# Kernel optimization log

Measured on AMD Instinct MI355X. Metric: run time of the kernel, lower is better.

## Reference

```python
import jax, jax.numpy as jnp
import numpy as np

C = 0.01          # Poincare ball curvature 1/100
SQRT_C = 0.1
EPS = 1e-15
BALL_EPS = 4e-3   # geoopt float32 projx boundary epsilon


def _norm(x):
    return jnp.linalg.norm(x, axis=-1, keepdims=True)


def expmap0(u):
    n = jnp.maximum(_norm(u), EPS)
    return jnp.tanh(SQRT_C * n) * u / (SQRT_C * n)


def logmap0(x):
    n = jnp.maximum(_norm(x), EPS)
    t = jnp.clip(SQRT_C * n, -1.0 + 1e-7, 1.0 - 1e-7)
    return jnp.arctanh(t) * x / (SQRT_C * n)


def projx(x):
    maxnorm = (1.0 - BALL_EPS) / SQRT_C
    n = jnp.maximum(_norm(x), EPS)
    return jnp.where(n > maxnorm, x / n * maxnorm, x)


def mobius_matvec(M, x):
    xn = jnp.maximum(_norm(x), EPS)
    mx = x @ M.T
    mxn = jnp.maximum(_norm(mx), EPS)
    t = jnp.clip(SQRT_C * xn, -1.0 + 1e-7, 1.0 - 1e-7)
    res = jnp.tanh(mxn / xn * jnp.arctanh(t)) * mx / (mxn * SQRT_C)
    return jnp.where(jnp.all(mx == 0, axis=-1, keepdims=True), 0.0, res)


def mobius_add(x, y):
    x2 = jnp.sum(x * x, -1, keepdims=True)
    y2 = jnp.sum(y * y, -1, keepdims=True)
    xy = jnp.sum(x * y, -1, keepdims=True)
    num = (1 + 2 * C * xy + C * y2) * x + (1 - C * x2) * y
    den = 1 + 2 * C * xy + C * C * x2 * y2
    return num / jnp.maximum(den, EPS)


def hyp_linear(x, W, b):
    # eval mode: weight dropout is a no-op
    res = projx(mobius_matvec(W, x))
    hb = projx(expmap0(b.reshape(1, -1)))
    return projx(mobius_add(res, hb))


def setup_inputs() -> dict:
    key = jax.random.key(0)
    ks = jax.random.split(key, 10)
    B, S, N, H, HEADS, E = 2, 4, 10000, 64, 4, 160000
    G = B * S
    OC = H // HEADS
    # edges guaranteed to have no self-loops (module removes then re-adds them)
    src = jax.random.randint(ks[0], (G, E), 0, N)
    off = jax.random.randint(ks[1], (G, E), 1, N)
    dst = (src + off) % N
    edge_index = jnp.stack([src, dst], axis=1).astype(jnp.int32)  # [G,2,E]

    def glorot(k, shape, fan):
        a = np.sqrt(6.0 / fan)
        return jax.random.uniform(k, shape, minval=-a, maxval=a, dtype=jnp.float32)

    emb = jax.random.normal(ks[2], (N, H), dtype=jnp.float32)
    att_i = glorot(ks[3], (1, HEADS, OC), HEADS * OC + 1)
    att_j = glorot(ks[4], (1, HEADS, OC), HEADS * OC + 1)
    w1 = glorot(ks[5], (H, OC), H + OC)   # HypLinear(in=16, out=64): weight [out,in]
    b1 = jnp.zeros((H,), jnp.float32)
    w2 = glorot(ks[6], (H, H), H + H)
    b2 = jnp.zeros((H,), jnp.float32)
    history_graphs = jnp.zeros((B, S, N), jnp.float32)  # only shape is used
    return {"history_graphs": history_graphs, "edge_index": edge_index,
            "emb": emb, "att_i": att_i, "att_j": att_j,
            "w1": w1, "b1": b1, "w2": w2, "b2": b2}


def reference(history_graphs, edge_index, emb, att_i, att_j, w1, b1, w2, b2):
    B, S, N = history_graphs.shape
    G = edge_index.shape[0]
    H = emb.shape[1]
    heads = att_i.shape[1]
    oc = H // heads

    # node ids are arange(N) for every (b,s) -> identical features per graph
    x0 = projx(expmap0(emb))   # initHyperX, [N,H]
    xt = logmap0(x0)           # tangent features used by attention, [N,H]

    # add self loops (inputs contain none)
    loops = jnp.broadcast_to(jnp.arange(N, dtype=edge_index.dtype)[None, None, :], (G, 2, N))
    ei = jnp.concatenate([edge_index, loops], axis=-1)  # [G,2,E+N]

    def agg(e):
        src, dst = e[0], e[1]                       # targets (i), sources (j)
        x_i = xt[src].reshape(-1, heads, oc)        # [E2,h,oc]
        x_j = xt[dst].reshape(-1, heads, oc)
        alpha = jnp.sum(x_i * att_i, -1) + jnp.sum(x_j * att_j, -1)  # [E2,h]
        alpha = jax.nn.leaky_relu(alpha, 0.2)
        m = jax.ops.segment_max(alpha, src, num_segments=N)
        a = jnp.exp(alpha - m[src])
        s = jax.ops.segment_sum(a, src, num_segments=N)
        a = a / (s[src] + 1e-16)                    # edge softmax; dropout eval no-op
        sup = jax.ops.segment_sum(x_j * a[..., None], src, num_segments=N)  # [N,h,oc]
        sup = sup.mean(axis=1)                      # concat=False -> head mean, [N,oc]
        return projx(expmap0(sup))

    h = jax.vmap(agg)(ei)                           # [G,N,oc]
    node_emb = h.reshape(B, S, N, oc)[:, -1]        # last timestep, [B,N,oc]

    z = hyp_linear(node_emb, w1, b1)                # 16 -> 64
    z = projx(expmap0(jax.nn.silu(logmap0(z))))     # HypAct(SiLU)
    z = projx(expmap0(logmap0(z)))                  # HypDropout (eval: log/exp round trip)
    z = hyp_linear(z, w2, b2)                       # 64 -> 64
    return z
```

## Files before the change

kernel.cpp:

```cpp
#include <hip/hip_runtime.h>
#include <hip/hip_bf16.h>

#define N_NODES 10000
#define NE 160000
#define CAP 96
#define SQRT_C 0.1f
#define RINV_SQRT_C 10.0f
#define CC 0.01f
#define EPS 1e-15f
#define MAXNORM ((1.0f - 4e-3f) / SQRT_C)
#define RMAXNORM (1.0f / MAXNORM)

__device__ __forceinline__ float frcp(float x) { return __builtin_amdgcn_rcpf(x); }
__device__ __forceinline__ float frsq(float x) { return __builtin_amdgcn_rsqf(x); }

__device__ __forceinline__ float fexp(float x) { return __expf(x); }
__device__ __forceinline__ float ftanh_pos(float x) {
    return 1.0f - 2.0f * frcp(__expf(2.0f * x) + 1.0f);
}
__device__ __forceinline__ float fatanh01(float t) {
    return 0.5f * __logf((1.0f + t) * frcp(1.0f - t));
}

__device__ __forceinline__ float ldf(const void* p, int i, int isbf) {
    return isbf ? __bfloat162float(((const __hip_bfloat16*)p)[i])
                : ((const float*)p)[i];
}

__device__ __forceinline__ int sniff_wave(const void* emb, int tid) {
    unsigned wv = ((const unsigned*)emb)[tid & 63];
    unsigned ex = (wv >> 7) & 0xFFu;
    unsigned long long m = __ballot(ex >= 116u && ex <= 133u);
    return (__popcll(m) >= 32) ? 1 : 0;
}

__device__ __forceinline__ float wsum(float v) {
#pragma unroll
    for (int off = 32; off > 0; off >>= 1) v += __shfl_xor(v, off, 64);
    return v;
}
__device__ __forceinline__ float wmax(float v) {
#pragma unroll
    for (int off = 32; off > 0; off >>= 1) v = fmaxf(v, __shfl_xor(v, off, 64));
    return v;
}

__device__ __forceinline__ float dpp_wsum(float x) {
    int t;
    t = __builtin_amdgcn_update_dpp(0, __float_as_int(x), 0x111, 0xF, 0xF, true);
    x += __int_as_float(t);
    t = __builtin_amdgcn_update_dpp(0, __float_as_int(x), 0x112, 0xF, 0xF, true);
    x += __int_as_float(t);
    t = __builtin_amdgcn_update_dpp(0, __float_as_int(x), 0x114, 0xF, 0xE, true);
    x += __int_as_float(t);
    t = __builtin_amdgcn_update_dpp(0, __float_as_int(x), 0x118, 0xF, 0xC, true);
    x += __int_as_float(t);
    t = __builtin_amdgcn_update_dpp(0, __float_as_int(x), 0x142, 0xA, 0xF, true);
    x += __int_as_float(t);
    t = __builtin_amdgcn_update_dpp(0, __float_as_int(x), 0x143, 0xC, 0xF, true);
    x += __int_as_float(t);
    return __int_as_float(__builtin_amdgcn_readlane(__float_as_int(x), 63));
}

__global__ __launch_bounds__(256) void pre_scatter(const void* __restrict__ emb,
                                                   const void* __restrict__ att_i,
                                                   const void* __restrict__ att_j,
                                                   const void* __restrict__ w1g,
                                                   const void* __restrict__ b1g,
                                                   const void* __restrict__ w2g,
                                                   const void* __restrict__ b2g,
                                                   const int* __restrict__ ei,
                                                   float* __restrict__ xt,
                                                   float* __restrict__ ai,
                                                   float* __restrict__ aj,
                                                   int* __restrict__ cnt,
                                                   unsigned short* __restrict__ bucket,
                                                   int* __restrict__ ovf_cnt,
                                                   unsigned* __restrict__ ovf,
                                                   int* __restrict__ flag,
                                                   float* __restrict__ wf1t,
                                                   float* __restrict__ wf2t,
                                                   float* __restrict__ hb1f,
                                                   float* __restrict__ hb2f,
                                                   float* __restrict__ hbn2) {
    __shared__ int sflag;
    int tid = threadIdx.x;
    int w = tid >> 6, lane = tid & 63;
    if (blockIdx.x < 2500) {
        if (tid < 64) { int s = sniff_wave(emb, tid); if (tid == 0) sflag = s; }
        __syncthreads();
        int isbf = sflag;
        int t = blockIdx.x * 256 + tid;
        int node = t >> 6;
        float u = ldf(emb, node * 64 + lane, isbf);
        float n2c = fmaxf(wsum(u * u), 1e-30f);
        float rn = frsq(n2c);
        float n = n2c * rn;
        float th = ftanh_pos(SQRT_C * n);
        float x0 = th * RINV_SQRT_C * rn * u;
        float x0n = th * RINV_SQRT_C;
        if (x0n > MAXNORM) { x0 *= MAXNORM * frcp(x0n); x0n = MAXNORM; }
        float tc = fminf(SQRT_C * x0n, 1.0f - 1e-7f);
        float xv = fatanh01(tc) * RINV_SQRT_C * frcp(x0n) * x0;
        xt[node * 64 + lane] = xv;
        float pi = xv * ldf(att_i, lane, isbf);
        float pj = xv * ldf(att_j, lane, isbf);
#pragma unroll
        for (int off = 8; off > 0; off >>= 1) {
            pi += __shfl_xor(pi, off, 64);
            pj += __shfl_xor(pj, off, 64);
        }
        if ((lane & 15) == 0) {
            ai[node * 4 + (lane >> 4)] = pi;
            aj[node * 4 + (lane >> 4)] = pj;
        }
    } else if (blockIdx.x < 2813) {
        int e0 = (blockIdx.x - 2500) * 512 + tid;
#pragma unroll
        for (int q = 0; q < 2; ++q) {
            int e = e0 + q * 256;
            if (e >= NE) break;
            int s0 = ei[3 * 2 * NE + e], d0 = ei[3 * 2 * NE + NE + e];
            int s1 = ei[7 * 2 * NE + e], d1 = ei[7 * 2 * NE + NE + e];
            int i0 = s0, i1 = N_NODES + s1;
            int p0 = atomicAdd(&cnt[i0], 1);
            int p1 = atomicAdd(&cnt[i1], 1);
            if (p0 < CAP) bucket[i0 * CAP + p0] = (unsigned short)d0;
            else {
                int oi = atomicAdd(ovf_cnt, 1);
                ovf[oi] = (0u << 28) | ((unsigned)s0 << 14) | (unsigned)d0;
            }
            if (p1 < CAP) bucket[i1 * CAP + p1] = (unsigned short)d1;
            else {
                int oi = atomicAdd(ovf_cnt, 1);
                ovf[oi] = (1u << 28) | ((unsigned)s1 << 14) | (unsigned)d1;
            }
        }
    } else {
        if (tid < 64) { int s = sniff_wave(emb, tid); if (tid == 0) sflag = s; }
        __syncthreads();
        int isbf = sflag;
        if (tid == 0) *flag = isbf;
        for (int i = tid; i < 1024; i += 256) {
            int o = i >> 4, c = i & 15;
            wf1t[c * 64 + o] = ldf(w1g, i, isbf);
        }
        for (int i = tid; i < 4096; i += 256) {
            int o = i >> 6, c = i & 63;
            wf2t[c * 64 + o] = ldf(w2g, i, isbf);
        }
        if (w < 2) {
            const void* bg = w ? b2g : b1g;
            float b = ldf(bg, lane, isbf);
            float n2c = fmaxf(wsum(b * b), 1e-30f);
            float rn = frsq(n2c);
            float n = n2c * rn;
            float th = ftanh_pos(SQRT_C * n);
            float hv = th * RINV_SQRT_C * rn * b;
            float hn = th * RINV_SQRT_C;
            if (hn > MAXNORM) { hv *= MAXNORM * frcp(hn); hn = MAXNORM; }
            (w ? hb2f : hb1f)[lane] = hv;
            if (lane == 0) hbn2[w] = hn * hn;
        }
    }
}

__global__ __launch_bounds__(256) void agg_head(const int* __restrict__ cnt,
                                                const unsigned short* __restrict__ bucket,
                                                const int* __restrict__ ovf_cnt,
                                                const unsigned* __restrict__ ovf,
                                                const float* __restrict__ ai,
                                                const float* __restrict__ aj,
                                                const float* __restrict__ xt,
                                                const float* __restrict__ wf1t,
                                                const float* __restrict__ wf2t,
                                                const float* __restrict__ hb1f,
                                                const float* __restrict__ hb2f,
                                                const float* __restrict__ hbn2,
                                                const int* __restrict__ flag,
                                                void* __restrict__ outv) {
    __shared__ float wlds[4][64 * 4];
    __shared__ int dlds[4][64];
    int w = threadIdx.x >> 6, lane = threadIdx.x & 63;
    int idx = blockIdx.x * 4 + w;
    int slot = (idx >= N_NODES) ? 1 : 0;
    int n = idx - slot * N_NODES;
    int deg = cnt[idx];
    int start = idx * CAP;

    float4 ai4 = *(const float4*)&ai[n * 4];
    float4 aj4n = *(const float4*)&aj[n * 4];
    float ain[4] = {ai4.x, ai4.y, ai4.z, ai4.w};
    float ajn[4] = {aj4n.x, aj4n.y, aj4n.z, aj4n.w};
    int hh = lane >> 4;
    float acc;

    if (deg <= 63) {
        bool act = (lane <= deg);
        int d = (lane < deg) ? (int)bucket[start + lane] : n;
        float4 a4 = act ? *(const float4*)&aj[d * 4] : make_float4(0.f, 0.f, 0.f, 0.f);
        float ajv[4] = {a4.x, a4.y, a4.z, a4.w};
        float eh[4];
#pragma unroll
        for (int h = 0; h < 4; ++h) {
            float a = ain[h] + ajv[h];
            a = (a < 0.0f) ? 0.2f * a : a;
            eh[h] = act ? fexp(a) : 0.0f;
        }
        float sh[4];
#pragma unroll
        for (int h = 0; h < 4; ++h) sh[h] = wsum(eh[h]);
#pragma unroll
        for (int h = 0; h < 4; ++h)
            wlds[w][lane * 4 + h] = eh[h] * (0.25f * frcp(sh[h] + 1e-16f));
        dlds[w][lane] = d;
        int m = deg + 1;
        float s0 = 0.f, s1 = 0.f, s2 = 0.f, s3 = 0.f;
        float s4 = 0.f, s5 = 0.f, s6 = 0.f, s7 = 0.f;
        int e = 0;
        for (; e + 8 <= m; e += 8) {
            int d0 = dlds[w][e],     d1 = dlds[w][e + 1];
            int d2 = dlds[w][e + 2], d3 = dlds[w][e + 3];
            int d4 = dlds[w][e + 4], d5 = dlds[w][e + 5];
            int d6 = dlds[w][e + 6], d7 = dlds[w][e + 7];
            float w0 = wlds[w][(e + 0) * 4 + hh], w1 = wlds[w][(e + 1) * 4 + hh];
            float w2 = wlds[w][(e + 2) * 4 + hh], w3 = wlds[w][(e + 3) * 4 + hh];
            float w4 = wlds[w][(e + 4) * 4 + hh], w5 = wlds[w][(e + 5) * 4 + hh];
            float w6 = wlds[w][(e + 6) * 4 + hh], w7 = wlds[w][(e + 7) * 4 + hh];
            s0 = fmaf(w0, xt[d0 * 64 + lane], s0);
            s1 = fmaf(w1, xt[d1 * 64 + lane], s1);
            s2 = fmaf(w2, xt[d2 * 64 + lane], s2);
            s3 = fmaf(w3, xt[d3 * 64 + lane], s3);
            s4 = fmaf(w4, xt[d4 * 64 + lane], s4);
            s5 = fmaf(w5, xt[d5 * 64 + lane], s5);
            s6 = fmaf(w6, xt[d6 * 64 + lane], s6);
            s7 = fmaf(w7, xt[d7 * 64 + lane], s7);
        }
        for (; e + 4 <= m; e += 4) {
            int d0 = dlds[w][e],     d1 = dlds[w][e + 1];
            int d2 = dlds[w][e + 2], d3 = dlds[w][e + 3];
            float w0 = wlds[w][(e + 0) * 4 + hh], w1 = wlds[w][(e + 1) * 4 + hh];
            float w2 = wlds[w][(e + 2) * 4 + hh], w3 = wlds[w][(e + 3) * 4 + hh];
            s0 = fmaf(w0, xt[d0 * 64 + lane], s0);
            s1 = fmaf(w1, xt[d1 * 64 + lane], s1);
            s2 = fmaf(w2, xt[d2 * 64 + lane], s2);
            s3 = fmaf(w3, xt[d3 * 64 + lane], s3);
        }
        for (; e < m; ++e)
            s0 = fmaf(wlds[w][e * 4 + hh], xt[dlds[w][e] * 64 + lane], s0);
        acc = ((s0 + s1) + (s2 + s3)) + ((s4 + s5) + (s6 + s7));
    } else {
        int bdeg = (deg < CAP) ? deg : CAP;
        int tov = (deg > CAP) ? *ovf_cnt : 0;
        float mh[4];
#pragma unroll
        for (int h = 0; h < 4; ++h) {
            float a = ain[h] + ajn[h];
            mh[h] = (a < 0.0f) ? 0.2f * a : a;
        }
        for (int e = lane; e < bdeg; e += 64) {
            int d = bucket[start + e];
#pragma unroll
            for (int h = 0; h < 4; ++h) {
                float a = ain[h] + aj[d * 4 + h];
                a = (a < 0.0f) ? 0.2f * a : a;
                mh[h] = fmaxf(mh[h], a);
            }
        }
        for (int k = lane; k < tov; k += 64) {
            unsigned pe = ovf[k];
            if ((int)(pe >> 28) == slot && (int)((pe >> 14) & 0x3FFFu) == n) {
                int d = pe & 0x3FFFu;
#pragma unroll
                for (int h = 0; h < 4; ++h) {
                    float a = ain[h] + aj[d * 4 + h];
                    a = (a < 0.0f) ? 0.2f * a : a;
                    mh[h] = fmaxf(mh[h], a);
                }
            }
        }
#pragma unroll
        for (int h = 0; h < 4; ++h) mh[h] = wmax(mh[h]);
        float sh[4] = {0.f, 0.f, 0.f, 0.f};
        if (lane == 0) {
#pragma unroll
            for (int h = 0; h < 4; ++h) {
                float a = ain[h] + ajn[h];
                a = (a < 0.0f) ? 0.2f * a : a;
                sh[h] = fexp(a - mh[h]);
            }
        }
        for (int e = lane; e < bdeg; e += 64) {
            int d = bucket[start + e];
#pragma unroll
            for (int h = 0; h < 4; ++h) {
                float a = ain[h] + aj[d * 4 + h];
                a = (a < 0.0f) ? 0.2f * a : a;
                sh[h] += fexp(a - mh[h]);
            }
        }
        for (int k = lane; k < tov; k += 64) {
            unsigned pe = ovf[k];
            if ((int)(pe >> 28) == slot && (int)((pe >> 14) & 0x3FFFu) == n) {
                int d = pe & 0x3FFFu;
#pragma unroll
                for (int h = 0; h < 4; ++h) {
                    float a = ain[h] + aj[d * 4 + h];
                    a = (a < 0.0f) ? 0.2f * a : a;
                    sh[h] += fexp(a - mh[h]);
                }
            }
        }
#pragma unroll
        for (int h = 0; h < 4; ++h) sh[h] = wsum(sh[h]);
        float scale[4];
#pragma unroll
        for (int h = 0; h < 4; ++h) scale[h] = 0.25f * frcp(sh[h] + 1e-16f);
        float aih = ain[hh], mhh = mh[hh], sch = scale[hh];
        float aself = aih + ajn[hh];
        aself = (aself < 0.0f) ? 0.2f * aself : aself;
        acc = fexp(aself - mhh) * sch * xt[n * 64 + lane];
        for (int e = 0; e < bdeg; ++e) {
            int d = bucket[start + e];
            float a = aih + aj[d * 4 + hh];
            a = (a < 0.0f) ? 0.2f * a : a;
            acc = fmaf(fexp(a - mhh) * sch, xt[d * 64 + lane], acc);
        }
        for (int k = 0; k < tov; ++k) {
            unsigned pe = ovf[k];
            if ((int)(pe >> 28) == slot && (int)((pe >> 14) & 0x3FFFu) == n) {
                int d = pe & 0x3FFFu;
                float a = aih + aj[d * 4 + hh];
                a = (a < 0.0f) ? 0.2f * a : a;
                acc = fmaf(fexp(a - mhh) * sch, xt[d * 64 + lane], acc);
            }
        }
    }
    acc += __shfl_xor(acc, 16, 64);
    acc += __shfl_xor(acc, 32, 64);

    float vl = acc;
    float* vbuf = wlds[w];
    float* zbuf = wlds[w] + 16;
    if (lane < 16) vbuf[lane] = vl;
    int isbf = *flag;
    float y2a = hbn2[0], y2b = hbn2[1];
    float hb1 = hb1f[lane], hb2v = hb2f[lane];

    float n2c = fmaxf(0.25f * dpp_wsum(vl * vl), 1e-30f);
    float rnv = frsq(n2c);
    float nn = n2c * rnv;
    float th0 = ftanh_pos(SQRT_C * nn);
    float s0v = th0 * RINV_SQRT_C * rnv;
    float x0n = th0 * RINV_SQRT_C;
    if (x0n > MAXNORM) { s0v *= MAXNORM * frcp(x0n); x0n = MAXNORM; }

    float a1 = 0.f;
#pragma unroll
    for (int j = 0; j < 4; ++j) {
        const float4 vq = *(const float4*)&vbuf[j * 4];
        a1 = fmaf(wf1t[(4 * j + 0) * 64 + lane], vq.x, a1);
        a1 = fmaf(wf1t[(4 * j + 1) * 64 + lane], vq.y, a1);
        a1 = fmaf(wf1t[(4 * j + 2) * 64 + lane], vq.z, a1);
        a1 = fmaf(wf1t[(4 * j + 3) * 64 + lane], vq.w, a1);
    }
    a1 *= s0v;

    float mxn2 = dpp_wsum(a1 * a1);
    float mxhb = dpp_wsum(a1 * hb1);
    float xn = fmaxf(x0n, EPS);
    float mxc = fmaxf(mxn2, 1e-30f);
    float rmx = frsq(mxc);
    float mxn = mxc * rmx;
    float t = fminf(SQRT_C * xn, 1.0f - 1e-7f);
    float th = ftanh_pos(mxn * frcp(xn) * fatanh01(t));
    float rs = th * RINV_SQRT_C * rmx;
    float rn = th * RINV_SQRT_C;
    if (mxn2 == 0.0f) { rs = 0.f; rn = 0.f; }
    if (rn > MAXNORM) { rs *= MAXNORM * frcp(rn); rn = MAXNORM; }
    float xy = rs * mxhb;
    float x2 = rn * rn;
    float A = 1.0f + 2.0f * CC * xy + CC * y2a;
    float B = 1.0f - CC * x2;
    float rden = frcp(fmaxf(1.0f + 2.0f * CC * xy + CC * CC * x2 * y2a, EPS));
    float z = (A * rs * a1 + B * hb1) * rden;

    float znc = fmaxf(dpp_wsum(z * z), 1e-30f);
    float rzn = frsq(znc);
    float zn = znc * rzn;
    float scz = (zn > MAXNORM) ? MAXNORM * rzn : 1.0f;
    float z1n = fminf(zn, MAXNORM);
    float rz1n = (zn > MAXNORM) ? RMAXNORM : rzn;
    float lg = fatanh01(fminf(SQRT_C * z1n, 1.0f - 1e-7f)) * RINV_SQRT_C * rz1n * scz;
    float u = lg * z;
    u = u * frcp(1.0f + __expf(-u));

    float unc = fmaxf(dpp_wsum(u * u), 1e-30f);
    float run = frsq(unc);
    float un = unc * run;
    float th2 = ftanh_pos(SQRT_C * un);
    float s2 = th2 * RINV_SQRT_C * run;
    float z2n = th2 * RINV_SQRT_C;
    if (z2n > MAXNORM) { s2 *= MAXNORM * frcp(z2n); z2n = MAXNORM; }
    float z2 = u * s2;

    zbuf[lane] = z2;
    float a2 = 0.f;
#pragma unroll
    for (int j = 0; j < 16; ++j) {
        const float4 zq = *(const float4*)&zbuf[j * 4];
        a2 = fmaf(wf2t[(4 * j + 0) * 64 + lane], zq.x, a2);
        a2 = fmaf(wf2t[(4 * j + 1) * 64 + lane], zq.y, a2);
        a2 = fmaf(wf2t[(4 * j + 2) * 64 + lane], zq.z, a2);
        a2 = fmaf(wf2t[(4 * j + 3) * 64 + lane], zq.w, a2);
    }

    float pn2 = dpp_wsum(a2 * a2);
    float ph2 = dpp_wsum(a2 * hb2v);
    float xnb = fmaxf(z2n, EPS);
    float pnc = fmaxf(pn2, 1e-30f);
    float rpx = frsq(pnc);
    float mxnb = pnc * rpx;
    float tb = fminf(SQRT_C * xnb, 1.0f - 1e-7f);
    float thb = ftanh_pos(mxnb * frcp(xnb) * fatanh01(tb));
    float rsb = thb * RINV_SQRT_C * rpx;
    float rnb = thb * RINV_SQRT_C;
    if (pn2 == 0.0f) { rsb = 0.f; rnb = 0.f; }
    if (rnb > MAXNORM) { rsb *= MAXNORM * frcp(rnb); rnb = MAXNORM; }
    float xyb = rsb * ph2;
    float x2b = rnb * rnb;
    float Ab = 1.0f + 2.0f * CC * xyb + CC * y2b;
    float Bb = 1.0f - CC * x2b;
    float rdenb = frcp(fmaxf(1.0f + 2.0f * CC * xyb + CC * CC * x2b * y2b, EPS));
    float zf = (Ab * rsb * a2 + Bb * hb2v) * rdenb;
    float zfc = fmaxf(dpp_wsum(zf * zf), 1e-30f);
    float rzf = frsq(zfc);
    float znf = zfc * rzf;
    float s4 = (znf > MAXNORM) ? MAXNORM * rzf : 1.0f;
    float val = zf * s4;

    if (isbf) ((__hip_bfloat16*)outv)[idx * 64 + lane] = __float2bfloat16(val);
    else      ((float*)outv)[idx * 64 + lane] = val;
}

extern "C" void kernel_launch(void* const* d_in, const int* in_sizes, int n_in,
                              void* d_out, int out_size, void* d_ws, size_t ws_size,
                              hipStream_t stream) {
    const int* ei = (const int*)d_in[1];
    const void* emb   = d_in[2];
    const void* att_i = d_in[3];
    const void* att_j = d_in[4];
    const void* w1 = d_in[5];
    const void* b1 = d_in[6];
    const void* w2 = d_in[7];
    const void* b2 = d_in[8];

    float* ws = (float*)d_ws;
    float* xt    = ws;
    float* ai    = ws + 640000;
    float* aj    = ws + 680000;
    int* cnt     = (int*)(ws + 1040000);
    int* ovf_cnt = (int*)(ws + 1060000);
    unsigned short* bucket = (unsigned short*)(ws + 1060032);
    unsigned* ovf = (unsigned*)(ws + 2020032);
    int* flag     = (int*)(ws + 2340032);
    float* wf1t = ws + 2340064;
    float* wf2t = ws + 2341088;
    float* hb1f = ws + 2345184;
    float* hb2f = ws + 2345248;
    float* hbn2 = ws + 2345312;

    hipMemsetAsync((void*)cnt, 0, (2 * N_NODES + 8) * sizeof(int), stream);
    hipLaunchKernelGGL(pre_scatter, dim3(2814), dim3(256), 0, stream,
                       emb, att_i, att_j, w1, b1, w2, b2, ei,
                       xt, ai, aj, cnt, bucket, ovf_cnt, ovf, flag,
                       wf1t, wf2t, hb1f, hb2f, hbn2);
    hipLaunchKernelGGL(agg_head, dim3(5000), dim3(256), 0, stream,
                       cnt, bucket, ovf_cnt, ovf, ai, aj, xt,
                       wf1t, wf2t, hb1f, hb2f, hbn2, flag, d_out);
}
```

Baseline: 129.4 us.

## Fuse pre-scatter and aggregation into one cooperative kernel with grid sync

Merges the two kernels into a single persistent cooperative kernel. Blocks grid-stride over the old pre-scatter work, meet at a grid-wide barrier, then grid-stride over the aggregation and head work. This removes one kernel launch and the inter-kernel gap, and passes the bf16 flag in shared memory instead of through global memory. In exchange it adds cooperative-launch and grid-sync overhead, an occupancy query on every call, and a grid capped by occupancy, which may reduce parallelism in the gather-heavy phase.

```diff
diff --git a/kernel.cpp b/kernel.cpp
--- a/kernel.cpp
+++ b/kernel.cpp
@@ -1,5 +1,8 @@
 #include <hip/hip_runtime.h>
 #include <hip/hip_bf16.h>
+#include <hip/hip_cooperative_groups.h>
+
+namespace cg = cooperative_groups;
 
 #define N_NODES 10000
 #define NE 160000
@@ -62,215 +65,191 @@
     return __int_as_float(__builtin_amdgcn_readlane(__float_as_int(x), 63));
 }
 
-__global__ __launch_bounds__(256) void pre_scatter(const void* __restrict__ emb,
-                                                   const void* __restrict__ att_i,
-                                                   const void* __restrict__ att_j,
-                                                   const void* __restrict__ w1g,
-                                                   const void* __restrict__ b1g,
-                                                   const void* __restrict__ w2g,
-                                                   const void* __restrict__ b2g,
-                                                   const int* __restrict__ ei,
-                                                   float* __restrict__ xt,
-                                                   float* __restrict__ ai,
-                                                   float* __restrict__ aj,
-                                                   int* __restrict__ cnt,
-                                                   unsigned short* __restrict__ bucket,
-                                                   int* __restrict__ ovf_cnt,
-                                                   unsigned* __restrict__ ovf,
-                                                   int* __restrict__ flag,
-                                                   float* __restrict__ wf1t,
-                                                   float* __restrict__ wf2t,
-                                                   float* __restrict__ hb1f,
-                                                   float* __restrict__ hb2f,
-                                                   float* __restrict__ hbn2) {
+__global__ __launch_bounds__(256, 4) void fused_all(const void* __restrict__ emb,
+                                                    const void* __restrict__ att_i,
+                                                    const void* __restrict__ att_j,
+                                                    const void* __restrict__ w1g,
+                                                    const void* __restrict__ b1g,
+                                                    const void* __restrict__ w2g,
+                                                    const void* __restrict__ b2g,
+                                                    const int* __restrict__ ei,
+                                                    float* __restrict__ xt,
+                                                    float* __restrict__ ai,
+                                                    float* __restrict__ aj,
+                                                    int* __restrict__ cnt,
+                                                    unsigned short* __restrict__ bucket,
+                                                    int* __restrict__ ovf_cnt,
+                                                    unsigned* __restrict__ ovf,
+                                                    float* __restrict__ wf1t,
+                                                    float* __restrict__ wf2t,
+                                                    float* __restrict__ hb1f,
+                                                    float* __restrict__ hb2f,
+                                                    float* __restrict__ hbn2,
+                                                    void* __restrict__ outv) {
+    __shared__ float wlds[4][64 * 4];
+    __shared__ int dlds[4][64];
     __shared__ int sflag;
     int tid = threadIdx.x;
     int w = tid >> 6, lane = tid & 63;
-    if (blockIdx.x < 2500) {
-        if (tid < 64) { int s = sniff_wave(emb, tid); if (tid == 0) sflag = s; }
-        __syncthreads();
-        int isbf = sflag;
-        int t = blockIdx.x * 256 + tid;
-        int node = t >> 6;
-        float u = ldf(emb, node * 64 + lane, isbf);
-        float n2c = fmaxf(wsum(u * u), 1e-30f);
-        float rn = frsq(n2c);
-        float n = n2c * rn;
-        float th = ftanh_pos(SQRT_C * n);
-        float x0 = th * RINV_SQRT_C * rn * u;
-        float x0n = th * RINV_SQRT_C;
-        if (x0n > MAXNORM) { x0 *= MAXNORM * frcp(x0n); x0n = MAXNORM; }
-        float tc = fminf(SQRT_C * x0n, 1.0f - 1e-7f);
-        float xv = fatanh01(tc) * RINV_SQRT_C * frcp(x0n) * x0;
-        xt[node * 64 + lane] = xv;
-        float pi = xv * ldf(att_i, lane, isbf);
-        float pj = xv * ldf(att_j, lane, isbf);
-#pragma unroll
-        for (int off = 8; off > 0; off >>= 1) {
-            pi += __shfl_xor(pi, off, 64);
-            pj += __shfl_xor(pj, off, 64);
-        }
-        if ((lane & 15) == 0) {
-            ai[node * 4 + (lane >> 4)] = pi;
-            aj[node * 4 + (lane >> 4)] = pj;
-        }
-    } else if (blockIdx.x < 2813) {
-        int e0 = (blockIdx.x - 2500) * 512 + tid;
-#pragma unroll
-        for (int q = 0; q < 2; ++q) {
-            int e = e0 + q * 256;
-            if (e >= NE) break;
-            int s0 = ei[3 * 2 * NE + e], d0 = ei[3 * 2 * NE + NE + e];
-            int s1 = ei[7 * 2 * NE + e], d1 = ei[7 * 2 * NE + NE + e];
-            int i0 = s0, i1 = N_NODES + s1;
-            int p0 = atomicAdd(&cnt[i0], 1);
-            int p1 = atomicAdd(&cnt[i1], 1);
-            if (p0 < CAP) bucket[i0 * CAP + p0] = (unsigned short)d0;
-            else {
-                int oi = atomicAdd(ovf_cnt, 1);
-                ovf[oi] = (0u << 28) | ((unsigned)s0 << 14) | (unsigned)d0;
-            }
-            if (p1 < CAP) bucket[i1 * CAP + p1] = (unsigned short)d1;
-            else {
-                int oi = atomicAdd(ovf_cnt, 1);
-                ovf[oi] = (1u << 28) | ((unsigned)s1 << 14) | (unsigned)d1;
-            }
-        }
-    } else {
-        if (tid < 64) { int s = sniff_wave(emb, tid); if (tid == 0) sflag = s; }
-        __syncthreads();
-        int isbf = sflag;
-        if (tid == 0) *flag = isbf;
-        for (int i = tid; i < 1024; i += 256) {
-            int o = i >> 4, c = i & 15;
-            wf1t[c * 64 + o] = ldf(w1g, i, isbf);
-        }
-        for (int i = tid; i < 4096; i += 256) {
-            int o = i >> 6, c = i & 63;
-            wf2t[c * 64 + o] = ldf(w2g, i, isbf);
-        }
-        if (w < 2) {
-            const void* bg = w ? b2g : b1g;
-            float b = ldf(bg, lane, isbf);
-            float n2c = fmaxf(wsum(b * b), 1e-30f);
+
+    if (tid < 64) { int s = sniff_wave(emb, tid); if (tid == 0) sflag = s; }
+    __syncthreads();
+    int isbf = sflag;
+
+    for (int b = blockIdx.x; b < 2814; b += gridDim.x) {
+        if (b < 2500) {
+            int t = b * 256 + tid;
+            int node = t >> 6;
+            float u = ldf(emb, node * 64 + lane, isbf);
+            float n2c = fmaxf(wsum(u * u), 1e-30f);
             float rn = frsq(n2c);
             float n = n2c * rn;
             float th = ftanh_pos(SQRT_C * n);
-            float hv = th * RINV_SQRT_C * rn * b;
-            float hn = th * RINV_SQRT_C;
-            if (hn > MAXNORM) { hv *= MAXNORM * frcp(hn); hn = MAXNORM; }
-            (w ? hb2f : hb1f)[lane] = hv;
-            if (lane == 0) hbn2[w] = hn * hn;
+            float x0 = th * RINV_SQRT_C * rn * u;
+            float x0n = th * RINV_SQRT_C;
+            if (x0n > MAXNORM) { x0 *= MAXNORM * frcp(x0n); x0n = MAXNORM; }
+            float tc = fminf(SQRT_C * x0n, 1.0f - 1e-7f);
+            float xv = fatanh01(tc) * RINV_SQRT_C * frcp(x0n) * x0;
+            xt[node * 64 + lane] = xv;
+            float pi = xv * ldf(att_i, lane, isbf);
+            float pj = xv * ldf(att_j, lane, isbf);
+#pragma unroll
+            for (int off = 8; off > 0; off >>= 1) {
+                pi += __shfl_xor(pi, off, 64);
+                pj += __shfl_xor(pj, off, 64);
+            }
+            if ((lane & 15) == 0) {
+                ai[node * 4 + (lane >> 4)] = pi;
+                aj[node * 4 + (lane >> 4)] = pj;
+            }
+        } else if (b < 2813) {
+            int e0 = (b - 2500) * 512 + tid;
+#pragma unroll
+            for (int q = 0; q < 2; ++q) {
+                int e = e0 + q * 256;
+                if (e >= NE) break;
+                int s0 = ei[3 * 2 * NE + e], d0 = ei[3 * 2 * NE + NE + e];
+                int s1 = ei[7 * 2 * NE + e], d1 = ei[7 * 2 * NE + NE + e];
+                int i0 = s0, i1 = N_NODES + s1;
+                int p0 = atomicAdd(&cnt[i0], 1);
+                int p1 = atomicAdd(&cnt[i1], 1);
+                if (p0 < CAP) bucket[i0 * CAP + p0] = (unsigned short)d0;
+                else {
+                    int oi = atomicAdd(ovf_cnt, 1);
+                    ovf[oi] = (0u << 28) | ((unsigned)s0 << 14) | (unsigned)d0;
+                }
+                if (p1 < CAP) bucket[i1 * CAP + p1] = (unsigned short)d1;
+                else {
+                    int oi = atomicAdd(ovf_cnt, 1);
+                    ovf[oi] = (1u << 28) | ((unsigned)s1 << 14) | (unsigned)d1;
+                }
+            }
+        } else {
+            for (int i = tid; i < 1024; i += 256) {
+                int o = i >> 4, c = i & 15;
+                wf1t[c * 64 + o] = ldf(w1g, i, isbf);
+            }
+            for (int i = tid; i < 4096; i += 256) {
+                int o = i >> 6, c = i & 63;
+                wf2t[c * 64 + o] = ldf(w2g, i, isbf);
+            }
+            if (w < 2) {
+                const void* bg = w ? b2g : b1g;
+                float bb = ldf(bg, lane, isbf);
+                float n2c = fmaxf(wsum(bb * bb), 1e-30f);
+                float rn = frsq(n2c);
+                float n = n2c * rn;
+                float th = ftanh_pos(SQRT_C * n);
+                float hv = th * RINV_SQRT_C * rn * bb;
+                float hn = th * RINV_SQRT_C;
+                if (hn > MAXNORM) { hv *= MAXNORM * frcp(hn); hn = MAXNORM; }
+                (w ? hb2f : hb1f)[lane] = hv;
+                if (lane == 0) hbn2[w] = hn * hn;
+            }
         }
     }
-}
-
-__global__ __launch_bounds__(256) void agg_head(const int* __restrict__ cnt,
-                                                const unsigned short* __restrict__ bucket,
-                                                const int* __restrict__ ovf_cnt,
-                                                const unsigned* __restrict__ ovf,
-                                                const float* __restrict__ ai,
-                                                const float* __restrict__ aj,
-                                                const float* __restrict__ xt,
-                                                const float* __restrict__ wf1t,
-                                                const float* __restrict__ wf2t,
-                                                const float* __restrict__ hb1f,
-                                                const float* __restrict__ hb2f,
-                                                const float* __restrict__ hbn2,
-                                                const int* __restrict__ flag,
-                                                void* __restrict__ outv) {
-    __shared__ float wlds[4][64 * 4];
-    __shared__ int dlds[4][64];
-    int w = threadIdx.x >> 6, lane = threadIdx.x & 63;
-    int idx = blockIdx.x * 4 + w;
-    int slot = (idx >= N_NODES) ? 1 : 0;
-    int n = idx - slot * N_NODES;
-    int deg = cnt[idx];
-    int start = idx * CAP;
-
-    float4 ai4 = *(const float4*)&ai[n * 4];
-    float4 aj4n = *(const float4*)&aj[n * 4];
-    float ain[4] = {ai4.x, ai4.y, ai4.z, ai4.w};
-    float ajn[4] = {aj4n.x, aj4n.y, aj4n.z, aj4n.w};
-    int hh = lane >> 4;
-    float acc;
-
-    if (deg <= 63) {
-        bool act = (lane <= deg);
-        int d = (lane < deg) ? (int)bucket[start + lane] : n;
-        float4 a4 = act ? *(const float4*)&aj[d * 4] : make_float4(0.f, 0.f, 0.f, 0.f);
-        float ajv[4] = {a4.x, a4.y, a4.z, a4.w};
-        float eh[4];
-#pragma unroll
-        for (int h = 0; h < 4; ++h) {
-            float a = ain[h] + ajv[h];
-            a = (a < 0.0f) ? 0.2f * a : a;
-            eh[h] = act ? fexp(a) : 0.0f;
-        }
-        float sh[4];
-#pragma unroll
-        for (int h = 0; h < 4; ++h) sh[h] = wsum(eh[h]);
-#pragma unroll
-        for (int h = 0; h < 4; ++h)
-            wlds[w][lane * 4 + h] = eh[h] * (0.25f * frcp(sh[h] + 1e-16f));
-        dlds[w][lane] = d;
-        int m = deg + 1;
-        float s0 = 0.f, s1 = 0.f, s2 = 0.f, s3 = 0.f;
-        float s4 = 0.f, s5 = 0.f, s6 = 0.f, s7 = 0.f;
-        int e = 0;
-        for (; e + 8 <= m; e += 8) {
-            int d0 = dlds[w][e],     d1 = dlds[w][e + 1];
-            int d2 = dlds[w][e + 2], d3 = dlds[w][e + 3];
-            int d4 = dlds[w][e + 4], d5 = dlds[w][e + 5];
-            int d6 = dlds[w][e + 6], d7 = dlds[w][e + 7];
-            float w0 = wlds[w][(e + 0) * 4 + hh], w1 = wlds[w][(e + 1) * 4 + hh];
-            float w2 = wlds[w][(e + 2) * 4 + hh], w3 = wlds[w][(e + 3) * 4 + hh];
-            float w4 = wlds[w][(e + 4) * 4 + hh], w5 = wlds[w][(e + 5) * 4 + hh];
-            float w6 = wlds[w][(e + 6) * 4 + hh], w7 = wlds[w][(e + 7) * 4 + hh];
-            s0 = fmaf(w0, xt[d0 * 64 + lane], s0);
-            s1 = fmaf(w1, xt[d1 * 64 + lane], s1);
-            s2 = fmaf(w2, xt[d2 * 64 + lane], s2);
-            s3 = fmaf(w3, xt[d3 * 64 + lane], s3);
-            s4 = fmaf(w4, xt[d4 * 64 + lane], s4);
-            s5 = fmaf(w5, xt[d5 * 64 + lane], s5);
-            s6 = fmaf(w6, xt[d6 * 64 + lane], s6);
-            s7 = fmaf(w7, xt[d7 * 64 + lane], s7);
-        }
-        for (; e + 4 <= m; e += 4) {
-            int d0 = dlds[w][e],     d1 = dlds[w][e + 1];
-            int d2 = dlds[w][e + 2], d3 = dlds[w][e + 3];
-            float w0 = wlds[w][(e + 0) * 4 + hh], w1 = wlds[w][(e + 1) * 4 + hh];
-            float w2 = wlds[w][(e + 2) * 4 + hh], w3 = wlds[w][(e + 3) * 4 + hh];
-            s0 = fmaf(w0, xt[d0 * 64 + lane], s0);
-            s1 = fmaf(w1, xt[d1 * 64 + lane], s1);
-            s2 = fmaf(w2, xt[d2 * 64 + lane], s2);
-            s3 = fmaf(w3, xt[d3 * 64 + lane], s3);
-        }
-        for (; e < m; ++e)
-            s0 = fmaf(wlds[w][e * 4 + hh], xt[dlds[w][e] * 64 + lane], s0);
-        acc = ((s0 + s1) + (s2 + s3)) + ((s4 + s5) + (s6 + s7));
-    } else {
-        int bdeg = (deg < CAP) ? deg : CAP;
-        int tov = (deg > CAP) ? *ovf_cnt : 0;
-        float mh[4];
-#pragma unroll
-        for (int h = 0; h < 4; ++h) {
-            float a = ain[h] + ajn[h];
-            mh[h] = (a < 0.0f) ? 0.2f * a : a;
-        }
-        for (int e = lane; e < bdeg; e += 64) {
-            int d = bucket[start + e];
+
+    cg::this_grid().sync();
+
+    for (int b = blockIdx.x; b < 5000; b += gridDim.x) {
+        int idx = b * 4 + w;
+        int slot = (idx >= N_NODES) ? 1 : 0;
+        int n = idx - slot * N_NODES;
+        int deg = cnt[idx];
+        int start = idx * CAP;
+
+        float4 ai4 = *(const float4*)&ai[n * 4];
+        float4 aj4n = *(const float4*)&aj[n * 4];
+        float ain[4] = {ai4.x, ai4.y, ai4.z, ai4.w};
+        float ajn[4] = {aj4n.x, aj4n.y, aj4n.z, aj4n.w};
+        int hh = lane >> 4;
+        float acc;
+
+        if (deg <= 63) {
+            bool act = (lane <= deg);
+            int d = (lane < deg) ? (int)bucket[start + lane] : n;
+            float4 a4 = act ? *(const float4*)&aj[d * 4] : make_float4(0.f, 0.f, 0.f, 0.f);
+            float ajv[4] = {a4.x, a4.y, a4.z, a4.w};
+            float eh[4];
 #pragma unroll
             for (int h = 0; h < 4; ++h) {
-                float a = ain[h] + aj[d * 4 + h];
+                float a = ain[h] + ajv[h];
                 a = (a < 0.0f) ? 0.2f * a : a;
-                mh[h] = fmaxf(mh[h], a);
-            }
-        }
-        for (int k = lane; k < tov; k += 64) {
-            unsigned pe = ovf[k];
-            if ((int)(pe >> 28) == slot && (int)((pe >> 14) & 0x3FFFu) == n) {
-                int d = pe & 0x3FFFu;
+                eh[h] = act ? fexp(a) : 0.0f;
+            }
+            float sh[4];
+#pragma unroll
+            for (int h = 0; h < 4; ++h) sh[h] = wsum(eh[h]);
+#pragma unroll
+            for (int h = 0; h < 4; ++h)
+                wlds[w][lane * 4 + h] = eh[h] * (0.25f * frcp(sh[h] + 1e-16f));
+            dlds[w][lane] = d;
+            int m = deg + 1;
+            float s0 = 0.f, s1 = 0.f, s2 = 0.f, s3 = 0.f;
+            float s4 = 0.f, s5 = 0.f, s6 = 0.f, s7 = 0.f;
+            int e = 0;
+            for (; e + 8 <= m; e += 8) {
+                int d0 = dlds[w][e],     d1 = dlds[w][e + 1];
+                int d2 = dlds[w][e + 2], d3 = dlds[w][e + 3];
+                int d4 = dlds[w][e + 4], d5 = dlds[w][e + 5];
+                int d6 = dlds[w][e + 6], d7 = dlds[w][e + 7];
+                float w0 = wlds[w][(e + 0) * 4 + hh], w1 = wlds[w][(e + 1) * 4 + hh];
+                float w2 = wlds[w][(e + 2) * 4 + hh], w3 = wlds[w][(e + 3) * 4 + hh];
+                float w4 = wlds[w][(e + 4) * 4 + hh], w5 = wlds[w][(e + 5) * 4 + hh];
+                float w6 = wlds[w][(e + 6) * 4 + hh], w7 = wlds[w][(e + 7) * 4 + hh];
+                s0 = fmaf(w0, xt[d0 * 64 + lane], s0);
+                s1 = fmaf(w1, xt[d1 * 64 + lane], s1);
+                s2 = fmaf(w2, xt[d2 * 64 + lane], s2);
+                s3 = fmaf(w3, xt[d3 * 64 + lane], s3);
+                s4 = fmaf(w4, xt[d4 * 64 + lane], s4);
+                s5 = fmaf(w5, xt[d5 * 64 + lane], s5);
+                s6 = fmaf(w6, xt[d6 * 64 + lane], s6);
+                s7 = fmaf(w7, xt[d7 * 64 + lane], s7);
+            }
+            for (; e + 4 <= m; e += 4) {
+                int d0 = dlds[w][e],     d1 = dlds[w][e + 1];
+                int d2 = dlds[w][e + 2], d3 = dlds[w][e + 3];
+                float w0 = wlds[w][(e + 0) * 4 + hh], w1 = wlds[w][(e + 1) * 4 + hh];
+                float w2 = wlds[w][(e + 2) * 4 + hh], w3 = wlds[w][(e + 3) * 4 + hh];
+                s0 = fmaf(w0, xt[d0 * 64 + lane], s0);
+                s1 = fmaf(w1, xt[d1 * 64 + lane], s1);
+                s2 = fmaf(w2, xt[d2 * 64 + lane], s2);
+                s3 = fmaf(w3, xt[d3 * 64 + lane], s3);
+            }
+            for (; e < m; ++e)
+                s0 = fmaf(wlds[w][e * 4 + hh], xt[dlds[w][e] * 64 + lane], s0);
+            acc = ((s0 + s1) + (s2 + s3)) + ((s4 + s5) + (s6 + s7));
+        } else {
+            int bdeg = (deg < CAP) ? deg : CAP;
+            int tov = (deg > CAP) ? *ovf_cnt : 0;
+            float mh[4];
+#pragma unroll
+            for (int h = 0; h < 4; ++h) {
+                float a = ain[h] + ajn[h];
+                mh[h] = (a < 0.0f) ? 0.2f * a : a;
+            }
+            for (int e = lane; e < bdeg; e += 64) {
+                int d = bucket[start + e];
 #pragma unroll
                 for (int h = 0; h < 4; ++h) {
                     float a = ain[h] + aj[d * 4 + h];
@@ -278,31 +257,31 @@
                     mh[h] = fmaxf(mh[h], a);
                 }
             }
-        }
-#pragma unroll
-        for (int h = 0; h < 4; ++h) mh[h] = wmax(mh[h]);
-        float sh[4] = {0.f, 0.f, 0.f, 0.f};
-        if (lane == 0) {
-#pragma unroll
-            for (int h = 0; h < 4; ++h) {
-                float a = ain[h] + ajn[h];
-                a = (a < 0.0f) ? 0.2f * a : a;
-                sh[h] = fexp(a - mh[h]);
-            }
-        }
-        for (int e = lane; e < bdeg; e += 64) {
-            int d = bucket[start + e];
-#pragma unroll
-            for (int h = 0; h < 4; ++h) {
-                float a = ain[h] + aj[d * 4 + h];
-                a = (a < 0.0f) ? 0.2f * a : a;
-                sh[h] += fexp(a - mh[h]);
-            }
-        }
-        for (int k = lane; k < tov; k += 64) {
-            unsigned pe = ovf[k];
-            if ((int)(pe >> 28) == slot && (int)((pe >> 14) & 0x3FFFu) == n) {
-                int d = pe & 0x3FFFu;
+            for (int k = lane; k < tov; k += 64) {
+                unsigned pe = ovf[k];
+                if ((int)(pe >> 28) == slot && (int)((pe >> 14) & 0x3FFFu) == n) {
+                    int d = pe & 0x3FFFu;
+#pragma unroll
+                    for (int h = 0; h < 4; ++h) {
+                        float a = ain[h] + aj[d * 4 + h];
+                        a = (a < 0.0f) ? 0.2f * a : a;
+                        mh[h] = fmaxf(mh[h], a);
+                    }
+                }
+            }
+#pragma unroll
+            for (int h = 0; h < 4; ++h) mh[h] = wmax(mh[h]);
+            float sh[4] = {0.f, 0.f, 0.f, 0.f};
+            if (lane == 0) {
+#pragma unroll
+                for (int h = 0; h < 4; ++h) {
+                    float a = ain[h] + ajn[h];
+                    a = (a < 0.0f) ? 0.2f * a : a;
+                    sh[h] = fexp(a - mh[h]);
+                }
+            }
+            for (int e = lane; e < bdeg; e += 64) {
+                int d = bucket[start + e];
 #pragma unroll
                 for (int h = 0; h < 4; ++h) {
                     float a = ain[h] + aj[d * 4 + h];
@@ -310,137 +289,148 @@
                     sh[h] += fexp(a - mh[h]);
                 }
             }
-        }
-#pragma unroll
-        for (int h = 0; h < 4; ++h) sh[h] = wsum(sh[h]);
-        float scale[4];
-#pragma unroll
-        for (int h = 0; h < 4; ++h) scale[h] = 0.25f * frcp(sh[h] + 1e-16f);
-        float aih = ain[hh], mhh = mh[hh], sch = scale[hh];
-        float aself = aih + ajn[hh];
-        aself = (aself < 0.0f) ? 0.2f * aself : aself;
-        acc = fexp(aself - mhh) * sch * xt[n * 64 + lane];
-        for (int e = 0; e < bdeg; ++e) {
-            int d = bucket[start + e];
-            float a = aih + aj[d * 4 + hh];
-            a = (a < 0.0f) ? 0.2f * a : a;
-            acc = fmaf(fexp(a - mhh) * sch, xt[d * 64 + lane], acc);
-        }
-        for (int k = 0; k < tov; ++k) {
-            unsigned pe = ovf[k];
-            if ((int)(pe >> 28) == slot && (int)((pe >> 14) & 0x3FFFu) == n) {
-                int d = pe & 0x3FFFu;
+            for (int k = lane; k < tov; k += 64) {
+                unsigned pe = ovf[k];
+                if ((int)(pe >> 28) == slot && (int)((pe >> 14) & 0x3FFFu) == n) {
+                    int d = pe & 0x3FFFu;
+#pragma unroll
+                    for (int h = 0; h < 4; ++h) {
+                        float a = ain[h] + aj[d * 4 + h];
+                        a = (a < 0.0f) ? 0.2f * a : a;
+                        sh[h] += fexp(a - mh[h]);
+                    }
+                }
+            }
+#pragma unroll
+            for (int h = 0; h < 4; ++h) sh[h] = wsum(sh[h]);
+            float scale[4];
+#pragma unroll
+            for (int h = 0; h < 4; ++h) scale[h] = 0.25f * frcp(sh[h] + 1e-16f);
+            float aih = ain[hh], mhh = mh[hh], sch = scale[hh];
+            float aself = aih + ajn[hh];
+            aself = (aself < 0.0f) ? 0.2f * aself : aself;
+            acc = fexp(aself - mhh) * sch * xt[n * 64 + lane];
+            for (int e = 0; e < bdeg; ++e) {
+                int d = bucket[start + e];
                 float a = aih + aj[d * 4 + hh];
                 a = (a < 0.0f) ? 0.2f * a : a;
                 acc = fmaf(fexp(a - mhh) * sch, xt[d * 64 + lane], acc);
             }
+            for (int k = 0; k < tov; ++k) {
+                unsigned pe = ovf[k];
+                if ((int)(pe >> 28) == slot && (int)((pe >> 14) & 0x3FFFu) == n) {
+                    int d = pe & 0x3FFFu;
+                    float a = aih + aj[d * 4 + hh];
+                    a = (a < 0.0f) ? 0.2f * a : a;
+                    acc = fmaf(fexp(a - mhh) * sch, xt[d * 64 + lane], acc);
+                }
+            }
         }
+        acc += __shfl_xor(acc, 16, 64);
+        acc += __shfl_xor(acc, 32, 64);
+
+        float vl = acc;
+        float* vbuf = wlds[w];
+        float* zbuf = wlds[w] + 16;
+        if (lane < 16) vbuf[lane] = vl;
+        float y2a = hbn2[0], y2b = hbn2[1];
+        float hb1 = hb1f[lane], hb2v = hb2f[lane];
+
+        float n2c = fmaxf(0.25f * dpp_wsum(vl * vl), 1e-30f);
+        float rnv = frsq(n2c);
+        float nn = n2c * rnv;
+        float th0 = ftanh_pos(SQRT_C * nn);
+        float s0v = th0 * RINV_SQRT_C * rnv;
+        float x0n = th0 * RINV_SQRT_C;
+        if (x0n > MAXNORM) { s0v *= MAXNORM * frcp(x0n); x0n = MAXNORM; }
+
+        float a1 = 0.f;
+#pragma unroll
+        for (int j = 0; j < 4; ++j) {
+            const float4 vq = *(const float4*)&vbuf[j * 4];
+            a1 = fmaf(wf1t[(4 * j + 0) * 64 + lane], vq.x, a1);
+            a1 = fmaf(wf1t[(4 * j + 1) * 64 + lane], vq.y, a1);
+            a1 = fmaf(wf1t[(4 * j + 2) * 64 + lane], vq.z, a1);
+            a1 = fmaf(wf1t[(4 * j + 3) * 64 + lane], vq.w, a1);
+        }
+        a1 *= s0v;
+
+        float mxn2 = dpp_wsum(a1 * a1);
+        float mxhb = dpp_wsum(a1 * hb1);
+        float xn = fmaxf(x0n, EPS);
+        float mxc = fmaxf(mxn2, 1e-30f);
+        float rmx = frsq(mxc);
+        float mxn = mxc * rmx;
+        float t = fminf(SQRT_C * xn, 1.0f - 1e-7f);
+        float th = ftanh_pos(mxn * frcp(xn) * fatanh01(t));
+        float rs = th * RINV_SQRT_C * rmx;
+        float rn = th * RINV_SQRT_C;
+        if (mxn2 == 0.0f) { rs = 0.f; rn = 0.f; }
+        if (rn > MAXNORM) { rs *= MAXNORM * frcp(rn); rn = MAXNORM; }
+        float xy = rs * mxhb;
+        float x2 = rn * rn;
+        float A = 1.0f + 2.0f * CC * xy + CC * y2a;
+        float B = 1.0f - CC * x2;
+        float rden = frcp(fmaxf(1.0f + 2.0f * CC * xy + CC * CC * x2 * y2a, EPS));
+        float z = (A * rs * a1 + B * hb1) * rden;
+
+        float znc = fmaxf(dpp_wsum(z * z), 1e-30f);
+        float rzn = frsq(znc);
+        float zn = znc * rzn;
+        float scz = (zn > MAXNORM) ? MAXNORM * rzn : 1.0f;
+        float z1n = fminf(zn, MAXNORM);
+        float rz1n = (zn > MAXNORM) ? RMAXNORM : rzn;
+        float lg = fatanh01(fminf(SQRT_C * z1n, 1.0f - 1e-7f)) * RINV_SQRT_C * rz1n * scz;
+        float u = lg * z;
+        u = u * frcp(1.0f + __expf(-u));
+
+        float unc = fmaxf(dpp_wsum(u * u), 1e-30f);
+        float run = frsq(unc);
+        float un = unc * run;
+        float th2 = ftanh_pos(SQRT_C * un);
+        float s2 = th2 * RINV_SQRT_C * run;
+        float z2n = th2 * RINV_SQRT_C;
+        if (z2n > MAXNORM) { s2 *= MAXNORM * frcp(z2n); z2n = MAXNORM; }
+        float z2 = u * s2;
+
+        zbuf[lane] = z2;
+        float a2 = 0.f;
+#pragma unroll
+        for (int j = 0; j < 16; ++j) {
+            const float4 zq = *(const float4*)&zbuf[j * 4];
+            a2 = fmaf(wf2t[(4 * j + 0) * 64 + lane], zq.x, a2);
+            a2 = fmaf(wf2t[(4 * j + 1) * 64 + lane], zq.y, a2);
+            a2 = fmaf(wf2t[(4 * j + 2) * 64 + lane], zq.z, a2);
+            a2 = fmaf(wf2t[(4 * j + 3) * 64 + lane], zq.w, a2);
+        }
+
+        float pn2 = dpp_wsum(a2 * a2);
+        float ph2 = dpp_wsum(a2 * hb2v);
+        float xnb = fmaxf(z2n, EPS);
+        float pnc = fmaxf(pn2, 1e-30f);
+        float rpx = frsq(pnc);
+        float mxnb = pnc * rpx;
+        float tb = fminf(SQRT_C * xnb, 1.0f - 1e-7f);
+        float thb = ftanh_pos(mxnb * frcp(xnb) * fatanh01(tb));
+        float rsb = thb * RINV_SQRT_C * rpx;
+        float rnb = thb * RINV_SQRT_C;
+        if (pn2 == 0.0f) { rsb = 0.f; rnb = 0.f; }
+        if (rnb > MAXNORM) { rsb *= MAXNORM * frcp(rnb); rnb = MAXNORM; }
+        float xyb = rsb * ph2;
+        float x2b = rnb * rnb;
+        float Ab = 1.0f + 2.0f * CC * xyb + CC * y2b;
+        float Bb = 1.0f - CC * x2b;
+        float rdenb = frcp(fmaxf(1.0f + 2.0f * CC * xyb + CC * CC * x2b * y2b, EPS));
+        float zf = (Ab * rsb * a2 + Bb * hb2v) * rdenb;
+        float zfc = fmaxf(dpp_wsum(zf * zf), 1e-30f);
+        float rzf = frsq(zfc);
+        float znf = zfc * rzf;
+        float s4 = (znf > MAXNORM) ? MAXNORM * rzf : 1.0f;
+        float val = zf * s4;
+
+        if (isbf) ((__hip_bfloat16*)outv)[idx * 64 + lane] = __float2bfloat16(val);
+        else      ((float*)outv)[idx * 64 + lane] = val;
     }
-    acc += __shfl_xor(acc, 16, 64);
-    acc += __shfl_xor(acc, 32, 64);
-
-    float vl = acc;
-    float* vbuf = wlds[w];
-    float* zbuf = wlds[w] + 16;
-    if (lane < 16) vbuf[lane] = vl;
-    int isbf = *flag;
-    float y2a = hbn2[0], y2b = hbn2[1];
-    float hb1 = hb1f[lane], hb2v = hb2f[lane];
-
-    float n2c = fmaxf(0.25f * dpp_wsum(vl * vl), 1e-30f);
-    float rnv = frsq(n2c);
-    float nn = n2c * rnv;
-    float th0 = ftanh_pos(SQRT_C * nn);
-    float s0v = th0 * RINV_SQRT_C * rnv;
-    float x0n = th0 * RINV_SQRT_C;
-    if (x0n > MAXNORM) { s0v *= MAXNORM * frcp(x0n); x0n = MAXNORM; }
-
-    float a1 = 0.f;
-#pragma unroll
-    for (int j = 0; j < 4; ++j) {
-        const float4 vq = *(const float4*)&vbuf[j * 4];
-        a1 = fmaf(wf1t[(4 * j + 0) * 64 + lane], vq.x, a1);
-        a1 = fmaf(wf1t[(4 * j + 1) * 64 + lane], vq.y, a1);
-        a1 = fmaf(wf1t[(4 * j + 2) * 64 + lane], vq.z, a1);
-        a1 = fmaf(wf1t[(4 * j + 3) * 64 + lane], vq.w, a1);
-    }
-    a1 *= s0v;
-
-    float mxn2 = dpp_wsum(a1 * a1);
-    float mxhb = dpp_wsum(a1 * hb1);
-    float xn = fmaxf(x0n, EPS);
-    float mxc = fmaxf(mxn2, 1e-30f);
-    float rmx = frsq(mxc);
-    float mxn = mxc * rmx;
-    float t = fminf(SQRT_C * xn, 1.0f - 1e-7f);
-    float th = ftanh_pos(mxn * frcp(xn) * fatanh01(t));
-    float rs = th * RINV_SQRT_C * rmx;
-    float rn = th * RINV_SQRT_C;
-    if (mxn2 == 0.0f) { rs = 0.f; rn = 0.f; }
-    if (rn > MAXNORM) { rs *= MAXNORM * frcp(rn); rn = MAXNORM; }
-    float xy = rs * mxhb;
-    float x2 = rn * rn;
-    float A = 1.0f + 2.0f * CC * xy + CC * y2a;
-    float B = 1.0f - CC * x2;
-    float rden = frcp(fmaxf(1.0f + 2.0f * CC * xy + CC * CC * x2 * y2a, EPS));
-    float z = (A * rs * a1 + B * hb1) * rden;
-
-    float znc = fmaxf(dpp_wsum(z * z), 1e-30f);
-    float rzn = frsq(znc);
-    float zn = znc * rzn;
-    float scz = (zn > MAXNORM) ? MAXNORM * rzn : 1.0f;
-    float z1n = fminf(zn, MAXNORM);
-    float rz1n = (zn > MAXNORM) ? RMAXNORM : rzn;
-    float lg = fatanh01(fminf(SQRT_C * z1n, 1.0f - 1e-7f)) * RINV_SQRT_C * rz1n * scz;
-    float u = lg * z;
-    u = u * frcp(1.0f + __expf(-u));
-
-    float unc = fmaxf(dpp_wsum(u * u), 1e-30f);
-    float run = frsq(unc);
-    float un = unc * run;
-    float th2 = ftanh_pos(SQRT_C * un);
-    float s2 = th2 * RINV_SQRT_C * run;
-    float z2n = th2 * RINV_SQRT_C;
-    if (z2n > MAXNORM) { s2 *= MAXNORM * frcp(z2n); z2n = MAXNORM; }
-    float z2 = u * s2;
-
-    zbuf[lane] = z2;
-    float a2 = 0.f;
-#pragma unroll
-    for (int j = 0; j < 16; ++j) {
-        const float4 zq = *(const float4*)&zbuf[j * 4];
-        a2 = fmaf(wf2t[(4 * j + 0) * 64 + lane], zq.x, a2);
-        a2 = fmaf(wf2t[(4 * j + 1) * 64 + lane], zq.y, a2);
-        a2 = fmaf(wf2t[(4 * j + 2) * 64 + lane], zq.z, a2);
-        a2 = fmaf(wf2t[(4 * j + 3) * 64 + lane], zq.w, a2);
-    }
-
-    float pn2 = dpp_wsum(a2 * a2);
-    float ph2 = dpp_wsum(a2 * hb2v);
-    float xnb = fmaxf(z2n, EPS);
-    float pnc = fmaxf(pn2, 1e-30f);
-    float rpx = frsq(pnc);
-    float mxnb = pnc * rpx;
-    float tb = fminf(SQRT_C * xnb, 1.0f - 1e-7f);
-    float thb = ftanh_pos(mxnb * frcp(xnb) * fatanh01(tb));
-    float rsb = thb * RINV_SQRT_C * rpx;
-    float rnb = thb * RINV_SQRT_C;
-    if (pn2 == 0.0f) { rsb = 0.f; rnb = 0.f; }
-    if (rnb > MAXNORM) { rsb *= MAXNORM * frcp(rnb); rnb = MAXNORM; }
-    float xyb = rsb * ph2;
-    float x2b = rnb * rnb;
-    float Ab = 1.0f + 2.0f * CC * xyb + CC * y2b;
-    float Bb = 1.0f - CC * x2b;
-    float rdenb = frcp(fmaxf(1.0f + 2.0f * CC * xyb + CC * CC * x2b * y2b, EPS));
-    float zf = (Ab * rsb * a2 + Bb * hb2v) * rdenb;
-    float zfc = fmaxf(dpp_wsum(zf * zf), 1e-30f);
-    float rzf = frsq(zfc);
-    float znf = zfc * rzf;
-    float s4 = (znf > MAXNORM) ? MAXNORM * rzf : 1.0f;
-    float val = zf * s4;
-
-    if (isbf) ((__hip_bfloat16*)outv)[idx * 64 + lane] = __float2bfloat16(val);
-    else      ((float*)outv)[idx * 64 + lane] = val;
 }
 
 extern "C" void kernel_launch(void* const* d_in, const int* in_sizes, int n_in,
@@ -463,7 +453,6 @@
     int* ovf_cnt = (int*)(ws + 1060000);
     unsigned short* bucket = (unsigned short*)(ws + 1060032);
     unsigned* ovf = (unsigned*)(ws + 2020032);
-    int* flag     = (int*)(ws + 2340032);
     float* wf1t = ws + 2340064;
     float* wf2t = ws + 2341088;
     float* hb1f = ws + 2345184;
@@ -471,11 +460,21 @@
     float* hbn2 = ws + 2345312;
 
     hipMemsetAsync((void*)cnt, 0, (2 * N_NODES + 8) * sizeof(int), stream);
-    hipLaunchKernelGGL(pre_scatter, dim3(2814), dim3(256), 0, stream,
-                       emb, att_i, att_j, w1, b1, w2, b2, ei,
-                       xt, ai, aj, cnt, bucket, ovf_cnt, ovf, flag,
-                       wf1t, wf2t, hb1f, hb2f, hbn2);
-    hipLaunchKernelGGL(agg_head, dim3(5000), dim3(256), 0, stream,
-                       cnt, bucket, ovf_cnt, ovf, ai, aj, xt,
-                       wf1t, wf2t, hb1f, hb2f, hbn2, flag, d_out);
-}
+
+    int blocksPerCU = 0;
+    if (hipOccupancyMaxActiveBlocksPerMultiprocessor(&blocksPerCU,
+            (const void*)fused_all, 256, 0) != hipSuccess || blocksPerCU < 1)
+        blocksPerCU = 2;
+    int grid = blocksPerCU * 256;
+    if (grid > 2048) grid = 2048;
+
+    void* outp = d_out;
+    void* args[] = { (void*)&emb, (void*)&att_i, (void*)&att_j,
+                     (void*)&w1, (void*)&b1, (void*)&w2, (void*)&b2,
+                     (void*)&ei, (void*)&xt, (void*)&ai, (void*)&aj,
+                     (void*)&cnt, (void*)&bucket, (void*)&ovf_cnt, (void*)&ovf,
+                     (void*)&wf1t, (void*)&wf2t, (void*)&hb1f, (void*)&hb2f,
+                     (void*)&hbn2, (void*)&outp };
+    hipLaunchCooperativeKernel((const void*)fused_all, dim3(grid), dim3(256),
+                               args, 0, stream);
+}
```

Measured after the change: 273.1 us. +111.0%, slower.
